# Performance work log

Measured on AMD Instinct MI355X. Metric: run time of the kernel, lower is better.

## Reference

```python
import jax, jax.numpy as jnp
import numpy as np

B, H, W, C = 8, 56, 56, 2048
NUM_HEADS = 8
WINDOW = 7  # partition/merge is identity for this per-token op; kept for documentation
D = C // NUM_HEADS  # 256


def setup_inputs() -> dict:
    key = jax.random.key(0)
    kx, kw = jax.random.split(key)
    x = jax.random.normal(kx, (B, H, W, C), dtype=jnp.float32)
    # per-head square weight, as in nn.Parameter(torch.randn(num_heads, d, d))
    weight = jax.random.normal(kw, (NUM_HEADS, D, D), dtype=jnp.float32)
    return {"x": x, "weight": weight}


def reference(x, weight):
    # Swin-style window partition -> per-head linear on each token -> window merge.
    # Partition and merge are exact inverse layout permutations, so the math
    # reduces to a per-token, per-head d x d matmul over the channel dim.
    b, h, w, c = x.shape
    n_heads, d, _ = weight.shape
    xh = x.reshape(b, h, w, n_heads, d)
    out = jnp.einsum('bhwnd,nde->bhwne', xh, weight)  # grouped small GEMM
    return out.reshape(b, h, w, c)
```

## Files before the change

### kernel.cpp

```cpp
#include <hip/hip_runtime.h>
#include <hip/hip_bf16.h>
#include <cstdint>

typedef __attribute__((ext_vector_type(8))) short v8s;
typedef __attribute__((ext_vector_type(4))) float v4f;

#define NUM_HEADS 8
#define D 256
#define CCH 2048
#define STRIPS 32
#define TILES 49

__device__ __forceinline__ short f2bf(float f) {
  unsigned u = __builtin_bit_cast(unsigned, f);
  u = (u + 0x7FFFu + ((u >> 16) & 1u)) >> 16;
  return (short)u;
}

__global__ __launch_bounds__(256) void pack_w(const float* __restrict__ w,
                                              short* __restrict__ p) {
  int idx  = blockIdx.x * 256 + threadIdx.x;
  int lane = idx & 63;
  int j    = (idx >> 6) & 15;
  int s    = (idx >> 10) & 7;
  int head = idx >> 13;
  int n  = j * 16 + (lane & 15);
  int k0 = s * 32 + (lane >> 4) * 8;
  const float* src = w + head * 65536 + k0 * 256 + n;
  v8s v;
#pragma unroll
  for (int e = 0; e < 8; ++e) v[e] = f2bf(src[e * 256]);
  *reinterpret_cast<v8s*>(p + (size_t)idx * 8) = v;
}

typedef __attribute__((address_space(1))) const unsigned int GAS;
typedef __attribute__((address_space(3))) unsigned int LAS;

__global__ __launch_bounds__(1024, 4) void grouped_mm(const float* __restrict__ x,
                                                      const short* __restrict__ pB,
                                                      float* __restrict__ out) {
  __shared__ alignas(16) char As[65536];
  const int tid  = threadIdx.x;
  const int wv   = tid >> 6;
  const int lane = tid & 63;
  const int mt   = wv & 1;
  const int ng   = wv >> 1;
  const int head  = blockIdx.x >> 5;
  const int strip = blockIdx.x & 31;

  const int arow = lane & 15;
  const int kg   = lane >> 4;

  v8s Bf0[8], Bf1[8];
  {
    const short* pb = pB + (size_t)head * 65536 + (size_t)lane * 8;
#pragma unroll
    for (int s = 0; s < 8; ++s) {
      Bf0[s] = *reinterpret_cast<const v8s*>(pb + (size_t)(s * 16 + 2 * ng)     * 512);
      Bf1[s] = *reinterpret_cast<const v8s*>(pb + (size_t)(s * 16 + 2 * ng + 1) * 512);
    }
  }

  const char* xbase = (const char*)(x + (size_t)strip * TILES * 16 * CCH + head * D);
  const unsigned swz = (unsigned)((wv & 7) << 4);
  const unsigned lsw = ((unsigned)(lane * 16)) ^ swz;

  auto stage = [&](int slot, int q, int t) {
    const char* g = xbase + ((size_t)(t * 16 + wv)) * (CCH * 4) ;
    char* l = As + (((slot * 2 + q) * 16 + wv) * 1024);
    __builtin_amdgcn_global_load_lds((GAS*)(g + lsw), (LAS*)l, 16, 0, 0);
  };

  stage(0, 0, 0);
  stage(0, 1, 1);
  __syncthreads();

  const unsigned rswz = (unsigned)((arow & 7) << 4);

  for (int p = 0; p < 25; ++p) {
    const int cur = p & 1;

    const int tn = 2 * p + 2;
    if (tn < TILES)     stage(cur ^ 1, 0, tn);
    if (tn + 1 < TILES) stage(cur ^ 1, 1, tn + 1);

    const int myt = 2 * p + mt;
    if (myt < TILES) {
      const char* ar = As + (((cur * 2 + mt) * 16 + arow) * 1024);
      v4f acc0 = (v4f){0.f, 0.f, 0.f, 0.f};
      v4f acc1 = (v4f){0.f, 0.f, 0.f, 0.f};
#pragma unroll
      for (int s = 0; s < 8; ++s) {
        const unsigned q0 = ((unsigned)(s * 128 + kg * 32)) ^ rswz;
        v4f lo = *reinterpret_cast<const v4f*>(ar + q0);
        v4f hi = *reinterpret_cast<const v4f*>(ar + (q0 ^ 16u));
        v8s af;
#pragma unroll
        for (int e = 0; e < 4; ++e) {
          af[e]     = f2bf(lo[e]);
          af[4 + e] = f2bf(hi[e]);
        }
        acc0 = __builtin_amdgcn_mfma_f32_16x16x32_bf16(af, Bf0[s], acc0, 0, 0, 0);
        acc1 = __builtin_amdgcn_mfma_f32_16x16x32_bf16(af, Bf1[s], acc1, 0, 0, 0);
      }
      float* op = out + (size_t)((strip * TILES + myt) * 16 + kg * 4) * CCH
                      + head * D + ng * 32 + (lane & 15);
#pragma unroll
      for (int r = 0; r < 4; ++r) {
        op[(size_t)r * CCH]      = acc0[r];
        op[(size_t)r * CCH + 16] = acc1[r];
      }
    }
    __syncthreads();
  }
}

extern "C" void kernel_launch(void* const* d_in, const int* in_sizes, int n_in,
                              void* d_out, int out_size, void* d_ws, size_t ws_size,
                              hipStream_t stream) {
  const float* x = (const float*)d_in[0];
  const float* w = (const float*)d_in[1];
  float* out = (float*)d_out;
  short* packed = (short*)d_ws;

  pack_w<<<256, 256, 0, stream>>>(w, packed);
  grouped_mm<<<NUM_HEADS * STRIPS, 1024, 0, stream>>>(x, packed, out);
}
```

Baseline: 88.04 us.

## Split grouped GEMM into 512 smaller blocks with one tile per iteration

Workgroups shrink from 1024 to 512 threads and the grid doubles from 256 to 512 blocks. Each block now owns a contiguous segment of 24 or 25 row tiles per head, processes one 16-row tile per iteration, and has each wave cover 32 output columns. This drops the old two-tiles-per-step scheme, the idle half-wave on the odd 49th tile, and cuts LDS to 32KB per block, aiming for better CU coverage and occupancy on the 256-CU part. The cost is that each block must load its full per-head B fragments, so weight-fragment loads per CU double, and there are more barriers per unit of work.

```diff
diff --git a/kernel.cpp b/kernel.cpp
--- a/kernel.cpp
+++ b/kernel.cpp
@@ -8,8 +8,8 @@
 #define NUM_HEADS 8
 #define D 256
 #define CCH 2048
-#define STRIPS 32
-#define TILES 49
+#define SEGS 64
+#define TILES_PER_HEAD 1568
 
 __device__ __forceinline__ short f2bf(float f) {
   unsigned u = __builtin_bit_cast(unsigned, f);
@@ -36,17 +36,17 @@
 typedef __attribute__((address_space(1))) const unsigned int GAS;
 typedef __attribute__((address_space(3))) unsigned int LAS;
 
-__global__ __launch_bounds__(1024, 4) void grouped_mm(const float* __restrict__ x,
-                                                      const short* __restrict__ pB,
-                                                      float* __restrict__ out) {
-  __shared__ alignas(16) char As[65536];
+__global__ __launch_bounds__(512, 4) void grouped_mm(const float* __restrict__ x,
+                                                     const short* __restrict__ pB,
+                                                     float* __restrict__ out) {
+  __shared__ alignas(16) char As[2][16384];
   const int tid  = threadIdx.x;
   const int wv   = tid >> 6;
   const int lane = tid & 63;
-  const int mt   = wv & 1;
-  const int ng   = wv >> 1;
-  const int head  = blockIdx.x >> 5;
-  const int strip = blockIdx.x & 31;
+  const int head = blockIdx.x >> 6;
+  const int seg  = blockIdx.x & 63;
+  const int t0   = (seg < 32) ? seg * 25 : 800 + (seg - 32) * 24;
+  const int nt   = (seg < 32) ? 25 : 24;
 
   const int arow = lane & 15;
   const int kg   = lane >> 4;
@@ -56,60 +56,58 @@
     const short* pb = pB + (size_t)head * 65536 + (size_t)lane * 8;
 #pragma unroll
     for (int s = 0; s < 8; ++s) {
-      Bf0[s] = *reinterpret_cast<const v8s*>(pb + (size_t)(s * 16 + 2 * ng)     * 512);
-      Bf1[s] = *reinterpret_cast<const v8s*>(pb + (size_t)(s * 16 + 2 * ng + 1) * 512);
+      Bf0[s] = *reinterpret_cast<const v8s*>(pb + (size_t)(s * 16 + 2 * wv)     * 512);
+      Bf1[s] = *reinterpret_cast<const v8s*>(pb + (size_t)(s * 16 + 2 * wv + 1) * 512);
     }
   }
 
-  const char* xbase = (const char*)(x + (size_t)strip * TILES * 16 * CCH + head * D);
-  const unsigned swz = (unsigned)((wv & 7) << 4);
-  const unsigned lsw = ((unsigned)(lane * 16)) ^ swz;
+  const char* xbase = (const char*)(x + (size_t)head * D);
 
-  auto stage = [&](int slot, int q, int t) {
-    const char* g = xbase + ((size_t)(t * 16 + wv)) * (CCH * 4) ;
-    char* l = As + (((slot * 2 + q) * 16 + wv) * 1024);
-    __builtin_amdgcn_global_load_lds((GAS*)(g + lsw), (LAS*)l, 16, 0, 0);
+  auto stage = [&](int slot, int t) {
+#pragma unroll
+    for (int q = 0; q < 2; ++q) {
+      const int r = 2 * wv + q;
+      const unsigned lsw = ((unsigned)(lane * 16)) ^ (unsigned)((r & 7) << 4);
+      const char* g = xbase + ((size_t)(t * 16 + r)) * (CCH * 4) + lsw;
+      char* l = As[slot] + r * 1024;
+      __builtin_amdgcn_global_load_lds((GAS*)g, (LAS*)l, 16, 0, 0);
+    }
   };
 
-  stage(0, 0, 0);
-  stage(0, 1, 1);
+  stage(0, t0);
   __syncthreads();
 
   const unsigned rswz = (unsigned)((arow & 7) << 4);
 
-  for (int p = 0; p < 25; ++p) {
+  for (int p = 0; p < nt; ++p) {
     const int cur = p & 1;
 
-    const int tn = 2 * p + 2;
-    if (tn < TILES)     stage(cur ^ 1, 0, tn);
-    if (tn + 1 < TILES) stage(cur ^ 1, 1, tn + 1);
+    if (p + 1 < nt) stage(cur ^ 1, t0 + p + 1);
 
-    const int myt = 2 * p + mt;
-    if (myt < TILES) {
-      const char* ar = As + (((cur * 2 + mt) * 16 + arow) * 1024);
-      v4f acc0 = (v4f){0.f, 0.f, 0.f, 0.f};
-      v4f acc1 = (v4f){0.f, 0.f, 0.f, 0.f};
+    const char* ar = As[cur] + arow * 1024;
+    v4f acc0 = (v4f){0.f, 0.f, 0.f, 0.f};
+    v4f acc1 = (v4f){0.f, 0.f, 0.f, 0.f};
 #pragma unroll
-      for (int s = 0; s < 8; ++s) {
-        const unsigned q0 = ((unsigned)(s * 128 + kg * 32)) ^ rswz;
-        v4f lo = *reinterpret_cast<const v4f*>(ar + q0);
-        v4f hi = *reinterpret_cast<const v4f*>(ar + (q0 ^ 16u));
-        v8s af;
+    for (int s = 0; s < 8; ++s) {
+      const unsigned q0 = ((unsigned)(s * 128 + kg * 32)) ^ rswz;
+      v4f lo = *reinterpret_cast<const v4f*>(ar + q0);
+      v4f hi = *reinterpret_cast<const v4f*>(ar + (q0 ^ 16u));
+      v8s af;
 #pragma unroll
-        for (int e = 0; e < 4; ++e) {
-          af[e]     = f2bf(lo[e]);
-          af[4 + e] = f2bf(hi[e]);
-        }
-        acc0 = __builtin_amdgcn_mfma_f32_16x16x32_bf16(af, Bf0[s], acc0, 0, 0, 0);
-        acc1 = __builtin_amdgcn_mfma_f32_16x16x32_bf16(af, Bf1[s], acc1, 0, 0, 0);
+      for (int e = 0; e < 4; ++e) {
+        af[e]     = f2bf(lo[e]);
+        af[4 + e] = f2bf(hi[e]);
       }
-      float* op = out + (size_t)((strip * TILES + myt) * 16 + kg * 4) * CCH
-                      + head * D + ng * 32 + (lane & 15);
+      acc0 = __builtin_amdgcn_mfma_f32_16x16x32_bf16(af, Bf0[s], acc0, 0, 0, 0);
+      acc1 = __builtin_amdgcn_mfma_f32_16x16x32_bf16(af, Bf1[s], acc1, 0, 0, 0);
+    }
+
+    float* op = out + (size_t)((t0 + p) * 16 + kg * 4) * CCH
+                    + head * D + wv * 32 + arow;
 #pragma unroll
-      for (int r = 0; r < 4; ++r) {
-        op[(size_t)r * CCH]      = acc0[r];
-        op[(size_t)r * CCH + 16] = acc1[r];
-      }
+    for (int r = 0; r < 4; ++r) {
+      op[(size_t)r * CCH]      = acc0[r];
+      op[(size_t)r * CCH + 16] = acc1[r];
     }
     __syncthreads();
   }
@@ -124,5 +122,5 @@
   short* packed = (short*)d_ws;
 
   pack_w<<<256, 256, 0, stream>>>(w, packed);
-  grouped_mm<<<NUM_HEADS * STRIPS, 1024, 0, stream>>>(x, packed, out);
+  grouped_mm<<<NUM_HEADS * SEGS, 512, 0, stream>>>(x, packed, out);
 }
```

Measured after the change: 89.38 us. Within noise of the previous version (+1.5%).
